# Optimization experiments

Hardware: AMD Instinct MI355X
Metric: run time of the kernel (lower is better)

## Reference

```python
import jax, jax.numpy as jnp
import numpy as np

N_NODES = 50000
N_EDGES = 800000
IN_F = 64
HID_F = 64
OUT_F = 12


def setup_inputs() -> dict:
    key = jax.random.key(0)
    ks = jax.random.split(key, 8)
    x = jax.random.normal(ks[0], (N_NODES, IN_F), dtype=jnp.float32)
    edge_index = jax.random.randint(ks[1], (2, N_EDGES), 0, N_NODES, dtype=jnp.int64)
    edge_attr = jax.random.uniform(ks[2], (N_EDGES, 1), dtype=jnp.float32)
    # Glorot-ish scaled weights
    W1 = jax.random.normal(ks[3], (IN_F, HID_F), dtype=jnp.float32) / np.sqrt(IN_F)
    b1 = jnp.zeros((HID_F,), dtype=jnp.float32)
    W2 = jax.random.normal(ks[4], (HID_F, HID_F), dtype=jnp.float32) / np.sqrt(HID_F)
    b2 = jnp.zeros((HID_F,), dtype=jnp.float32)
    Wfc = jax.random.normal(ks[5], (HID_F, OUT_F), dtype=jnp.float32) / np.sqrt(HID_F)
    bfc = jnp.zeros((OUT_F,), dtype=jnp.float32)
    return {"x": x, "edge_index": edge_index, "edge_attr": edge_attr,
            "W1": W1, "b1": b1, "W2": W2, "b2": b2, "Wfc": Wfc, "bfc": bfc}


def _gcn_conv(h, src, dst, ew, W, b, n_nodes):
    """PyG GCNConv: linear -> add self-loops (weight 1) -> sym-normalized scatter-add -> +bias."""
    hl = h @ W  # [N, F_out]
    loop = jnp.arange(n_nodes, dtype=src.dtype)
    s = jnp.concatenate([src, loop])
    d = jnp.concatenate([dst, loop])
    w = jnp.concatenate([ew, jnp.ones((n_nodes,), dtype=hl.dtype)])
    deg = jax.ops.segment_sum(w, d, num_segments=n_nodes)
    dinv = jnp.where(deg > 0, jax.lax.rsqrt(jnp.maximum(deg, 1e-30)), 0.0)
    norm = dinv[s] * w * dinv[d]  # per-edge coefficient
    out = jax.ops.segment_sum(norm[:, None] * hl[s], d, num_segments=n_nodes)
    return out + b


def reference(x, edge_index, edge_attr, W1, b1, W2, b2, Wfc, bfc):
    src, dst = edge_index[0], edge_index[1]
    ew = edge_attr.squeeze(-1)
    n = x.shape[0]
    h = jax.nn.relu(_gcn_conv(x, src, dst, ew, W1, b1, n))
    h = jax.nn.relu(_gcn_conv(h, src, dst, ew, W2, b2, n))
    return h @ Wfc + bfc
```

## Files before the change

### kernel.cpp

```cpp
#include <hip/hip_runtime.h>
#include <hip/hip_bf16.h>
#include <hip/hip_fp16.h>


#define N_FEAT   64
#define OUT_F    12
#define NTHREADS 256
#define MAXDEG   52
#define AGG_BLOCKS 2048
#define FIXS     1048576.0f
#define FIXINV   (1.0f / 1048576.0f)

struct Params {
    const float* x; const int* idx; const float* ew;
    const float* W1; const float* b1; const float* W2; const float* b2;
    const float* Wfc; const float* bfc;
    float* out;
    int n_nodes, n_edges;
    unsigned long long* deg64;
    float* dinv;
    unsigned int* ell;
    __hip_bfloat16* xbf;
    __hip_bfloat16* h1bf;
};

__device__ __forceinline__ float unpack_w(unsigned int e) {
    return __half2float(__ushort_as_half((unsigned short)(e & 0xffffu)));
}

__device__ __forceinline__ float ell_gather(const __hip_bfloat16* __restrict__ hl,
                                            const unsigned int* __restrict__ row,
                                            int cnt, int lane, float acc) {
    const int nq = cnt >> 2;
    if (nq > 0) {
        uint4 a = *(const uint4*)(row);
        float va0 = __bfloat162float(hl[(a.x >> 16) * 64 + lane]);
        float va1 = __bfloat162float(hl[(a.y >> 16) * 64 + lane]);
        float va2 = __bfloat162float(hl[(a.z >> 16) * 64 + lane]);
        float va3 = __bfloat162float(hl[(a.w >> 16) * 64 + lane]);
        uint4 b = (nq > 1) ? *(const uint4*)(row + 4) : a;
        for (int q = 1; q < nq; q++) {
            uint4 c = (q + 1 < nq) ? *(const uint4*)(row + 4 * (q + 1)) : b;
            float vb0 = __bfloat162float(hl[(b.x >> 16) * 64 + lane]);
            float vb1 = __bfloat162float(hl[(b.y >> 16) * 64 + lane]);
            float vb2 = __bfloat162float(hl[(b.z >> 16) * 64 + lane]);
            float vb3 = __bfloat162float(hl[(b.w >> 16) * 64 + lane]);
            acc += unpack_w(a.x) * va0;
            acc += unpack_w(a.y) * va1;
            acc += unpack_w(a.z) * va2;
            acc += unpack_w(a.w) * va3;
            a = b; va0 = vb0; va1 = vb1; va2 = vb2; va3 = vb3;
            b = c;
        }
        acc += unpack_w(a.x) * va0;
        acc += unpack_w(a.y) * va1;
        acc += unpack_w(a.z) * va2;
        acc += unpack_w(a.w) * va3;
    }
    for (int k = nq << 2; k < cnt; k++) {
        unsigned int e = row[k];
        acc += unpack_w(e) * __bfloat162float(hl[(e >> 16) * 64 + lane]);
    }
    return acc;
}


__global__ void kf_count(Params p) {
    int e2 = blockIdx.x * NTHREADS + threadIdx.x;
    int nE2 = p.n_edges >> 1;
    if (e2 < nE2) {
        int2   s2 = ((const int2*)p.idx)[e2];
        int2   d2 = ((const int2*)(p.idx + p.n_edges))[e2];
        float2 w2 = ((const float2*)p.ew)[e2];
        unsigned long long o0 =
            atomicAdd(&p.deg64[d2.x], (1ull << 44) | (unsigned long long)(w2.x * FIXS));
        unsigned long long o1 =
            atomicAdd(&p.deg64[d2.y], (1ull << 44) | (unsigned long long)(w2.y * FIXS));
        int sl0 = (int)(o0 >> 44);
        int sl1 = (int)(o1 >> 44);
        if (sl0 < MAXDEG)
            p.ell[d2.x * MAXDEG + sl0] = ((unsigned int)s2.x << 16) |
                                         (unsigned int)__half_as_ushort(__float2half(w2.x));
        if (sl1 < MAXDEG)
            p.ell[d2.y * MAXDEG + sl1] = ((unsigned int)s2.y << 16) |
                                         (unsigned int)__half_as_ushort(__float2half(w2.y));
    }
    if (e2 == 0 && (p.n_edges & 1)) {
        int e = p.n_edges - 1;
        int s = p.idx[e], d = p.idx[p.n_edges + e];
        float w = p.ew[e];
        unsigned long long o =
            atomicAdd(&p.deg64[d], (1ull << 44) | (unsigned long long)(w * FIXS));
        int sl = (int)(o >> 44);
        if (sl < MAXDEG)
            p.ell[d * MAXDEG + sl] =
                ((unsigned int)s << 16) | (unsigned int)__half_as_ushort(__float2half(w));
    }
}

__global__ void kf_scalex(Params p) {
    int t = threadIdx.x, b = blockIdx.x, nb = gridDim.x;
    int lane = t & 63;
    int wid  = t >> 6;
    for (int base = b * 4; base < p.n_nodes; base += nb * 4) {
        int node = base + wid;
        if (node < p.n_nodes) {
            unsigned long long dv = p.deg64[node];
            float di = rsqrtf((float)(dv & 0xFFFFFFFFFFFull) * FIXINV + 1.0f);
            float xv = p.x[node * 64 + lane];
            p.xbf[node * 64 + lane] = __float2bfloat16(di * xv);
            if (lane == 0) p.dinv[node] = di;
        }
    }
}

__global__ void kf_agg1g1(Params p) {
    __shared__ float Ws[64 * 64];
    __shared__ float hs[4][64];
    int t = threadIdx.x, b = blockIdx.x, nb = gridDim.x;
    {
        const float4* W4 = (const float4*)p.W1;
        float4* Ws4 = (float4*)Ws;
        for (int i = t; i < 1024; i += NTHREADS) Ws4[i] = W4[i];
    }
    __syncthreads();
    int lane = t & 63;
    int wid  = t >> 6;
    float bv = p.b1[lane];
    for (int base = b * 4; base < p.n_nodes; base += nb * 4) {
        int node = base + wid;
        float g = 0.f;
        float di = 0.f;
        if (node < p.n_nodes) {
            di = p.dinv[node];
            int cnt = (int)(p.deg64[node] >> 44);
            cnt = (cnt > MAXDEG) ? MAXDEG : cnt;
            float acc = __bfloat162float(p.xbf[node * 64 + lane]);
            acc = ell_gather(p.xbf, p.ell + (long long)node * MAXDEG, cnt, lane, acc);
            g = di * acc;
        }
        hs[wid][lane] = g;
        __syncthreads();
        float o = 0.f;
#pragma unroll
        for (int k4 = 0; k4 < 16; k4++) {
            float4 hv = *(const float4*)&hs[wid][k4 * 4];
            int kb = k4 << 2;
            o += hv.x * Ws[(kb + 0) * 64 + lane];
            o += hv.y * Ws[(kb + 1) * 64 + lane];
            o += hv.z * Ws[(kb + 2) * 64 + lane];
            o += hv.w * Ws[(kb + 3) * 64 + lane];
        }
        if (node < p.n_nodes) {
            float h1 = fmaxf(o + bv, 0.0f);
            p.h1bf[node * 64 + lane] = __float2bfloat16(di * h1);
        }
        __syncthreads();
    }
}

__global__ void kf_agg2fc(Params p) {
    __shared__ float Ws[64 * 64];
    __shared__ float Wf[64 * OUT_F];
    __shared__ float bf[OUT_F];
    __shared__ float hs[4][64];
    int t = threadIdx.x, b = blockIdx.x, nb = gridDim.x;
    {
        const float4* W4 = (const float4*)p.W2;
        float4* Ws4 = (float4*)Ws;
        for (int i = t; i < 1024; i += NTHREADS) Ws4[i] = W4[i];
    }
    for (int i = t; i < 64 * OUT_F; i += NTHREADS) Wf[i] = p.Wfc[i];
    if (t < OUT_F) bf[t] = p.bfc[t];
    __syncthreads();
    int lane = t & 63;
    int wid  = t >> 6;
    float bv = p.b2[lane];
    for (int base = b * 4; base < p.n_nodes; base += nb * 4) {
        int node = base + wid;
        float g = 0.f;
        if (node < p.n_nodes) {
            float di  = p.dinv[node];
            int   cnt = (int)(p.deg64[node] >> 44);
            cnt = (cnt > MAXDEG) ? MAXDEG : cnt;
            float acc = __bfloat162float(p.h1bf[node * 64 + lane]);
            acc = ell_gather(p.h1bf, p.ell + (long long)node * MAXDEG, cnt, lane, acc);
            g = di * acc;
        }
        hs[wid][lane] = g;
        __syncthreads();
        float o = 0.f;
#pragma unroll
        for (int k4 = 0; k4 < 16; k4++) {
            float4 hv = *(const float4*)&hs[wid][k4 * 4];
            int kb = k4 << 2;
            o += hv.x * Ws[(kb + 0) * 64 + lane];
            o += hv.y * Ws[(kb + 1) * 64 + lane];
            o += hv.z * Ws[(kb + 2) * 64 + lane];
            o += hv.w * Ws[(kb + 3) * 64 + lane];
        }
        float h2 = fmaxf(o + bv, 0.0f);
        hs[wid][lane] = h2;
        __syncthreads();
        if (t < 4 * OUT_F) {
            int nd = t / OUT_F;
            int c  = t - nd * OUT_F;
            int gnode = base + nd;
            if (gnode < p.n_nodes) {
                float o2 = bf[c];
                const float* hrow = hs[nd];
#pragma unroll
                for (int k = 0; k < 64; k++) o2 += hrow[k] * Wf[k * OUT_F + c];
                p.out[gnode * OUT_F + c] = o2;
            }
        }
        __syncthreads();
    }
}

extern "C" void kernel_launch(void* const* d_in, const int* in_sizes, int n_in,
                              void* d_out, int out_size, void* d_ws, size_t ws_size,
                              hipStream_t stream) {
    Params p;
    p.x   = (const float*)d_in[0];
    p.idx = (const int*)d_in[1];
    p.ew  = (const float*)d_in[2];
    p.W1  = (const float*)d_in[3];
    p.b1  = (const float*)d_in[4];
    p.W2  = (const float*)d_in[5];
    p.b2  = (const float*)d_in[6];
    p.Wfc = (const float*)d_in[7];
    p.bfc = (const float*)d_in[8];
    p.out = (float*)d_out;
    p.n_nodes = in_sizes[0] / N_FEAT;
    p.n_edges = in_sizes[2];

    float* ws = (float*)d_ws;
    p.deg64 = (unsigned long long*)ws;
    p.dinv  = ws + 100032;
    p.ell   = (unsigned int*)(ws + 150048);
    p.xbf   = (__hip_bfloat16*)(ws + 2750048);
    p.h1bf  = (__hip_bfloat16*)(ws + 4350048);

    int gE2 = (p.n_edges / 2 + NTHREADS - 1) / NTHREADS;

    (void)hipMemsetAsync(ws, 0, 100000u * 4u, stream);
    kf_count <<<gE2,        NTHREADS, 0, stream>>>(p);
    kf_scalex<<<AGG_BLOCKS, NTHREADS, 0, stream>>>(p);
    kf_agg1g1<<<AGG_BLOCKS, NTHREADS, 0, stream>>>(p);
    kf_agg2fc<<<AGG_BLOCKS, NTHREADS, 0, stream>>>(p);
}
```

Before: 238.9 us.

## Replace block barriers with per-wave LDS fences in aggregation kernels

Each wave now owns its own shared-memory row and processes nodes independently, so the block-wide __syncthreads calls are replaced with an s_waitcnt lgkmcnt(0) fence. This lets the four waves in a block run out of step instead of waiting for the slowest gather, which matters because node degrees vary. The final FC projection is now computed per wave by 12 lanes rather than by 48 threads of the block, and the aggregation grid size is lowered. The change relies on a wave executing in lockstep for correctness within its own LDS row.

```diff
diff --git a/kernel.cpp b/kernel.cpp
--- a/kernel.cpp
+++ b/kernel.cpp
@@ -7,7 +7,7 @@
 #define OUT_F    12
 #define NTHREADS 256
 #define MAXDEG   52
-#define AGG_BLOCKS 2048
+#define AGG_BLOCKS 1792
 #define FIXS     1048576.0f
 #define FIXINV   (1.0f / 1048576.0f)
 
@@ -26,6 +26,10 @@
 
 __device__ __forceinline__ float unpack_w(unsigned int e) {
     return __half2float(__ushort_as_half((unsigned short)(e & 0xffffu)));
+}
+
+__device__ __forceinline__ void lds_fence() {
+    asm volatile("s_waitcnt lgkmcnt(0)" ::: "memory");
 }
 
 __device__ __forceinline__ float ell_gather(const __hip_bfloat16* __restrict__ hl,
@@ -102,15 +106,12 @@
     int t = threadIdx.x, b = blockIdx.x, nb = gridDim.x;
     int lane = t & 63;
     int wid  = t >> 6;
-    for (int base = b * 4; base < p.n_nodes; base += nb * 4) {
-        int node = base + wid;
-        if (node < p.n_nodes) {
-            unsigned long long dv = p.deg64[node];
-            float di = rsqrtf((float)(dv & 0xFFFFFFFFFFFull) * FIXINV + 1.0f);
-            float xv = p.x[node * 64 + lane];
-            p.xbf[node * 64 + lane] = __float2bfloat16(di * xv);
-            if (lane == 0) p.dinv[node] = di;
-        }
+    for (int node = b * 4 + wid; node < p.n_nodes; node += nb * 4) {
+        unsigned long long dv = p.deg64[node];
+        float di = rsqrtf((float)(dv & 0xFFFFFFFFFFFull) * FIXINV + 1.0f);
+        float xv = p.x[node * 64 + lane];
+        p.xbf[node * 64 + lane] = __float2bfloat16(di * xv);
+        if (lane == 0) p.dinv[node] = di;
     }
 }
 
@@ -127,35 +128,28 @@
     int lane = t & 63;
     int wid  = t >> 6;
     float bv = p.b1[lane];
-    for (int base = b * 4; base < p.n_nodes; base += nb * 4) {
-        int node = base + wid;
-        float g = 0.f;
-        float di = 0.f;
-        if (node < p.n_nodes) {
-            di = p.dinv[node];
-            int cnt = (int)(p.deg64[node] >> 44);
-            cnt = (cnt > MAXDEG) ? MAXDEG : cnt;
-            float acc = __bfloat162float(p.xbf[node * 64 + lane]);
-            acc = ell_gather(p.xbf, p.ell + (long long)node * MAXDEG, cnt, lane, acc);
-            g = di * acc;
-        }
-        hs[wid][lane] = g;
-        __syncthreads();
+    float* hrow = hs[wid];
+    for (int node = b * 4 + wid; node < p.n_nodes; node += nb * 4) {
+        float di = p.dinv[node];
+        int cnt = (int)(p.deg64[node] >> 44);
+        cnt = (cnt > MAXDEG) ? MAXDEG : cnt;
+        float acc = __bfloat162float(p.xbf[node * 64 + lane]);
+        acc = ell_gather(p.xbf, p.ell + (long long)node * MAXDEG, cnt, lane, acc);
+        hrow[lane] = di * acc;
+        lds_fence();
         float o = 0.f;
 #pragma unroll
         for (int k4 = 0; k4 < 16; k4++) {
-            float4 hv = *(const float4*)&hs[wid][k4 * 4];
+            float4 hv = *(const float4*)&hrow[k4 * 4];
             int kb = k4 << 2;
             o += hv.x * Ws[(kb + 0) * 64 + lane];
             o += hv.y * Ws[(kb + 1) * 64 + lane];
             o += hv.z * Ws[(kb + 2) * 64 + lane];
             o += hv.w * Ws[(kb + 3) * 64 + lane];
         }
-        if (node < p.n_nodes) {
-            float h1 = fmaxf(o + bv, 0.0f);
-            p.h1bf[node * 64 + lane] = __float2bfloat16(di * h1);
-        }
-        __syncthreads();
+        float h1 = fmaxf(o + bv, 0.0f);
+        p.h1bf[node * 64 + lane] = __float2bfloat16(di * h1);
+        lds_fence();
     }
 }
 
@@ -176,23 +170,19 @@
     int lane = t & 63;
     int wid  = t >> 6;
     float bv = p.b2[lane];
-    for (int base = b * 4; base < p.n_nodes; base += nb * 4) {
-        int node = base + wid;
-        float g = 0.f;
-        if (node < p.n_nodes) {
-            float di  = p.dinv[node];
-            int   cnt = (int)(p.deg64[node] >> 44);
-            cnt = (cnt > MAXDEG) ? MAXDEG : cnt;
-            float acc = __bfloat162float(p.h1bf[node * 64 + lane]);
-            acc = ell_gather(p.h1bf, p.ell + (long long)node * MAXDEG, cnt, lane, acc);
-            g = di * acc;
-        }
-        hs[wid][lane] = g;
-        __syncthreads();
+    float* hrow = hs[wid];
+    for (int node = b * 4 + wid; node < p.n_nodes; node += nb * 4) {
+        float di  = p.dinv[node];
+        int   cnt = (int)(p.deg64[node] >> 44);
+        cnt = (cnt > MAXDEG) ? MAXDEG : cnt;
+        float acc = __bfloat162float(p.h1bf[node * 64 + lane]);
+        acc = ell_gather(p.h1bf, p.ell + (long long)node * MAXDEG, cnt, lane, acc);
+        hrow[lane] = di * acc;
+        lds_fence();
         float o = 0.f;
 #pragma unroll
         for (int k4 = 0; k4 < 16; k4++) {
-            float4 hv = *(const float4*)&hs[wid][k4 * 4];
+            float4 hv = *(const float4*)&hrow[k4 * 4];
             int kb = k4 << 2;
             o += hv.x * Ws[(kb + 0) * 64 + lane];
             o += hv.y * Ws[(kb + 1) * 64 + lane];
@@ -200,21 +190,23 @@
             o += hv.w * Ws[(kb + 3) * 64 + lane];
         }
         float h2 = fmaxf(o + bv, 0.0f);
-        hs[wid][lane] = h2;
-        __syncthreads();
-        if (t < 4 * OUT_F) {
-            int nd = t / OUT_F;
-            int c  = t - nd * OUT_F;
-            int gnode = base + nd;
-            if (gnode < p.n_nodes) {
-                float o2 = bf[c];
-                const float* hrow = hs[nd];
+        lds_fence();
+        hrow[lane] = h2;
+        lds_fence();
+        if (lane < OUT_F) {
+            float o2 = bf[lane];
 #pragma unroll
-                for (int k = 0; k < 64; k++) o2 += hrow[k] * Wf[k * OUT_F + c];
-                p.out[gnode * OUT_F + c] = o2;
+            for (int k4 = 0; k4 < 16; k4++) {
+                float4 hq = *(const float4*)&hrow[k4 * 4];
+                int kb = k4 << 2;
+                o2 += hq.x * Wf[(kb + 0) * OUT_F + lane];
+                o2 += hq.y * Wf[(kb + 1) * OUT_F + lane];
+                o2 += hq.z * Wf[(kb + 2) * OUT_F + lane];
+                o2 += hq.w * Wf[(kb + 3) * OUT_F + lane];
             }
-        }
-        __syncthreads();
+            p.out[node * OUT_F + lane] = o2;
+        }
+        lds_fence();
     }
 }
 
```

Measured after the change: 214.2 us. -10.3%, faster.
